# Kernel tuning notes

Hardware: AMD Instinct MI355X
Metric: run time of the kernel (lower is better)

Reference implementation:

```python
import jax, jax.numpy as jnp
import numpy as np

B, N, E, D, H = 128, 256, 1024, 128, 8
DK = D // H
NEG = -9e15

def _xavier(key, shape):
    lim = np.sqrt(6.0 / (shape[0] + shape[1]))
    return jax.random.uniform(key, shape, jnp.float32, -lim, lim)

def setup_inputs() -> dict:
    key = jax.random.key(0)
    ks = jax.random.split(key, 10)
    x = jax.random.normal(ks[0], (B, N, D), jnp.float32)
    mask = jax.random.randint(ks[1], (B, N), 0, 2) > 0
    mask = mask.at[:, 0].set(True)  # ensure no fully-masked molecule
    # unique (row, col) edges per molecule -> scatter .set matches torch index_put
    perm = jax.vmap(lambda k: jax.random.permutation(k, N * N)[:E])(jax.random.split(ks[2], B))
    edge_index = jnp.stack([perm // N, perm % N], axis=1).astype(jnp.int32)  # [B, 2, E]
    edge_attr = jax.random.normal(ks[3], (B, E, D), jnp.float32)
    return {
        "x": x, "mask": mask, "edge_index": edge_index, "edge_attr": edge_attr,
        "Wq": _xavier(ks[4], (D + 2, D)),
        "Wk": _xavier(ks[5], (D + 2, D)),
        "Wv": _xavier(ks[6], (D + 2, D)),
        "We_w": _xavier(ks[7], (D, D)),
        "We_b": jax.random.normal(ks[8], (D,), jnp.float32) * 0.02,
        "ln_g": jnp.ones((D,), jnp.float32),
        "ln_b": jnp.zeros((D,), jnp.float32),
    }

def reference(x, mask, edge_index, edge_attr, Wq, Wk, Wv, We_w, We_b, ln_g, ln_b):
    rows, cols = edge_index[:, 0, :], edge_index[:, 1, :]  # [B, E]
    # per-molecule degree features (torch_geometric.degree per row/col)
    deg = lambda idx: jax.vmap(lambda r: jnp.zeros((N,), x.dtype).at[r].add(1.0))(idx)
    deg_r, deg_c = deg(rows), deg(cols)
    x_new = jnp.concatenate([x, deg_r[..., None], deg_c[..., None]], axis=-1)  # [B,N,D+2]
    # edge bias: linear -> mean over features -> scatter into [B,N,N]
    edge_feats = (edge_attr @ We_w + We_b).mean(axis=-1)  # [B, E]
    edge_bias = jax.vmap(lambda r, c, f: jnp.zeros((N, N), x.dtype).at[r, c].set(f))(rows, cols, edge_feats)
    q = (x_new @ Wq).reshape(B, N, H, DK).transpose(0, 2, 1, 3)
    k = (x_new @ Wk).reshape(B, N, H, DK).transpose(0, 2, 1, 3)
    v = (x_new @ Wv).reshape(B, N, H, DK).transpose(0, 2, 1, 3)
    scores = jnp.einsum('bhqd,bhkd->bhqk', q, k) / np.sqrt(DK).astype(x.dtype)
    # mask keys first, then add edge bias (matches torch op order)
    scores = jnp.where(mask[:, None, None, :], scores, NEG) + edge_bias[:, None, :, :]
    attn = jax.nn.softmax(scores, axis=-1)  # dropout is identity in eval
    out = jnp.einsum('bhqk,bhkd->bhqd', attn, v).transpose(0, 2, 1, 3).reshape(B, N, D)
    out = out + x
    mu = out.mean(axis=-1, keepdims=True)
    var = out.var(axis=-1, keepdims=True)
    return (out - mu) / jnp.sqrt(var + 1e-6) * ln_g + ln_b
```

## Files before the change

kernel.cpp:

```cpp
#include <hip/hip_runtime.h>
#include <stdint.h>

#define NB 128
#define NN 256
#define NE 1024
#define ND 128
#define NH 8
#define NDK 16
#define NEGV -9.0e15f

typedef unsigned short u16;
typedef unsigned int u32;
typedef unsigned char u8;
typedef __attribute__((ext_vector_type(8))) short short8;
typedef __attribute__((ext_vector_type(4))) float float4v;
typedef __attribute__((ext_vector_type(2))) float f32x2;

__device__ __forceinline__ float bf2f(u16 u) { return __uint_as_float(((u32)u) << 16); }
__device__ __forceinline__ u16 f2bf(float f) {
    u32 u = __float_as_uint(f);
    u += 0x7fffu + ((u >> 16) & 1u);
    return (u16)(u >> 16);
}
__device__ __forceinline__ float ldf(const void* p, size_t i, int f32) {
    return f32 ? ((const float*)p)[i] : bf2f(((const u16*)p)[i]);
}
__device__ __forceinline__ void stf(void* p, size_t i, int f32, float v) {
    if (f32) ((float*)p)[i] = v;
    else ((u16*)p)[i] = f2bf(v);
}
__device__ __forceinline__ void unpack8(uint4 a, float* o) {
    o[0] = bf2f(a.x & 0xffff); o[1] = bf2f(a.x >> 16);
    o[2] = bf2f(a.y & 0xffff); o[3] = bf2f(a.y >> 16);
    o[4] = bf2f(a.z & 0xffff); o[5] = bf2f(a.z >> 16);
    o[6] = bf2f(a.w & 0xffff); o[7] = bf2f(a.w >> 16);
}
__device__ __forceinline__ f32x2 bfpair(u32 w) {
    return (f32x2){__uint_as_float(w << 16), __uint_as_float(w & 0xffff0000u)};
}
__device__ __forceinline__ u32 pk_bf(float a, float b) {
    return ((__float_as_uint(a) + 0x8000u) >> 16) |
           ((__float_as_uint(b) + 0x8000u) & 0xffff0000u);
}
union Pack8 { u16 u[8]; u32 w[4]; short8 v; };

__device__ __forceinline__ int wave_detect_f32(const u16* x16) {
    int lane = threadIdx.x & 63;
    uint4 a = *(const uint4*)(x16 + lane * 8);
    u32 w[4] = {a.x, a.y, a.z, a.w};
    u32 ev = 0;
#pragma unroll
    for (int j = 0; j < 4; ++j) {
        ev |= ((((w[j] & 0xffffu) >> 7) & 0xffu) >= 0xC2u) ? 1u : 0u;
        ev |= (((w[j] >> 23) & 0xffu) >= 0xC2u) ? 1u : 0u;
    }
#pragma unroll
    for (int off = 32; off; off >>= 1) ev |= (u32)__shfl_xor((int)ev, off, 64);
    return ev ? 1 : 0;
}
__device__ __forceinline__ int wave_detect_mw(const u8* m8) {
    int lane = threadIdx.x & 63;
    uint4 m = *(const uint4*)(m8 + lane * 16);
    u32 w[4] = {m.x, m.y, m.z, m.w};
    u32 g1 = 0, mx = 0;
#pragma unroll
    for (int j = 0; j < 4; ++j) {
        u32 b0 = w[j] & 0xffu, b1 = (w[j] >> 8) & 0xffu;
        u32 b2 = (w[j] >> 16) & 0xffu, b3 = w[j] >> 24;
        g1 |= b1;
        u32 ma = b0 > b1 ? b0 : b1, mb2 = b2 > b3 ? b2 : b3;
        u32 mc = ma > mb2 ? ma : mb2;
        mx = mx > mc ? mx : mc;
    }
#pragma unroll
    for (int off = 32; off; off >>= 1) {
        g1 |= (u32)__shfl_xor((int)g1, off, 64);
        u32 o = (u32)__shfl_xor((int)mx, off, 64);
        mx = mx > o ? mx : o;
    }
    return (g1 == 0) ? 4 : ((mx <= 1u) ? 1 : 2);
}

__global__ __launch_bounds__(64) void k_wpk(const u16* x16,
                                            const void* Wew, const void* Web,
                                            float* wmean,
                                            const void* Wq, const void* Wk,
                                            const void* Wv, u16* WP) {
    int f32 = wave_detect_f32(x16);
    int bid = blockIdx.x, lane = threadIdx.x;
    if (bid < 129) {
        int k = bid;
        const void* src = (k < 128) ? Wew : Web;
        size_t base = (k < 128) ? (size_t)k * ND : 0;
        float s = ldf(src, base + lane, f32) + ldf(src, base + lane + 64, f32);
#pragma unroll
        for (int off = 32; off; off >>= 1) s += __shfl_xor(s, off, 64);
        if (lane == 0) wmean[k] = s * (1.0f / ND);
    } else {
        int id = bid - 129;
        int kT = id / 24, nT = id % 24;
        int col = lane & 15, quad = lane >> 4;
        int n = nT * 16 + col;
        int mat = n >> 7, nm = n & 127;
        const void* W = (mat == 0) ? Wq : (mat == 1) ? Wk : Wv;
        Pack8 c;
#pragma unroll
        for (int j = 0; j < 8; ++j) {
            int k = kT * 32 + quad * 8 + j;
            c.u[j] = (k < 130) ? f2bf(ldf(W, (size_t)k * ND + nm, f32)) : (u16)0;
        }
        *(short8*)(WP + ((size_t)(kT * 24 + nT) * 64 + lane) * 8) = c.v;
    }
}

__global__ __launch_bounds__(256) void k_edge(const u16* x16, const void* ea,
                                              const float* wmean, const int* ei,
                                              float* degr, float* degc,
                                              int* rowstartG, u16* colsG,
                                              float* featsG) {
    __shared__ __align__(16) float swm[132];
    __shared__ float featsL[NE];
    __shared__ int cr[NN], cc[NN], offs[NN], rs[NN + 1];
    int b = blockIdx.x, tid = threadIdx.x;
    int f32 = wave_detect_f32(x16);
    if (tid <= ND) swm[tid] = wmean[tid];
    cr[tid] = 0; cc[tid] = 0;
    __syncthreads();
    {
        int sub = tid & 15, grp = tid >> 4;
        const float4* wv = (const float4*)&swm[sub * 8];
        float4 w0 = wv[0], w1 = wv[1];
        float wb = swm[ND];
        const size_t ebase = (size_t)b * NE;
#pragma unroll 4
        for (int t = 0; t < 64; ++t) {
            int e = t * 16 + grp;
            size_t base = (ebase + e) * ND + sub * 8;
            float part;
            if (f32) {
                const float4* p = (const float4*)((const float*)ea + base);
                float4 a0 = p[0], a1 = p[1];
                part = a0.x * w0.x + a0.y * w0.y + a0.z * w0.z + a0.w * w0.w +
                       a1.x * w1.x + a1.y * w1.y + a1.z * w1.z + a1.w * w1.w;
            } else {
                uint4 a = *(const uint4*)((const u16*)ea + base);
                float xv[8];
                unpack8(a, xv);
                part = xv[0] * w0.x + xv[1] * w0.y + xv[2] * w0.z + xv[3] * w0.w +
                       xv[4] * w1.x + xv[5] * w1.y + xv[6] * w1.z + xv[7] * w1.w;
            }
            part += __shfl_xor(part, 1);
            part += __shfl_xor(part, 2);
            part += __shfl_xor(part, 4);
            part += __shfl_xor(part, 8);
            if (sub == 0) featsL[e] = part + wb;
        }
    }
    const int* rows = ei + (size_t)b * 2 * NE;
    const int* cols = rows + NE;
    for (int e = tid; e < NE; e += 256) {
        atomicAdd(&cr[rows[e]], 1);
        atomicAdd(&cc[cols[e]], 1);
    }
    __syncthreads();
    degr[b * NN + tid] = (float)cr[tid];
    degc[b * NN + tid] = (float)cc[tid];
    if (tid == 0) {
        int a = 0;
        for (int n = 0; n < NN; ++n) { rs[n] = a; a += cr[n]; }
        rs[NN] = a;
    }
    __syncthreads();
    offs[tid] = rs[tid];
    rowstartG[b * (NN + 1) + tid] = rs[tid];
    if (tid == 0) rowstartG[b * (NN + 1) + NN] = rs[NN];
    __syncthreads();
    for (int e = tid; e < NE; e += 256) {
        int r = rows[e];
        int pos = atomicAdd(&offs[r], 1);
        colsG[(size_t)b * NE + pos] = (u16)cols[e];
        featsG[(size_t)b * NE + pos] = featsL[e];
    }
}

__global__ __launch_bounds__(256) void k_gemm(const void* x, const float* degr,
                                              const float* degc, const u16* WP,
                                              u16* qw, u16* kw,
                                              u16* vw, u16* vt) {
    int tid = threadIdx.x;
    int w = tid >> 6, lane = tid & 63;
    int quad = lane >> 4, col = lane & 15;
    int m0 = blockIdx.x * 64 + w * 16;
    int row = m0 + col;
    int f32 = wave_detect_f32((const u16*)x);

    float4v acc[24];
#pragma unroll
    for (int t = 0; t < 24; ++t) acc[t] = (float4v){0.f, 0.f, 0.f, 0.f};

    const short8* wp = (const short8*)WP;
    for (int kT = 0; kT < 5; ++kT) {
        short8 a;
        if (kT < 4) {
            if (!f32) {
                a = *(const short8*)((const u16*)x + (size_t)row * ND + kT * 32 + quad * 8);
            } else {
                const float* xf = (const float*)x + (size_t)row * ND + kT * 32 + quad * 8;
                Pack8 c;
#pragma unroll
                for (int j = 0; j < 8; ++j) c.u[j] = f2bf(xf[j]);
                a = c.v;
            }
        } else {
            Pack8 c;
#pragma unroll
            for (int j = 0; j < 8; ++j) c.u[j] = 0;
            if (quad == 0) {
                c.u[0] = f2bf(degr[row]);
                c.u[1] = f2bf(degc[row]);
            }
            a = c.v;
        }
#pragma unroll
        for (int nT = 0; nT < 24; ++nT) {
            short8 bfr = wp[(size_t)(kT * 24 + nT) * 64 + lane];
            acc[nT] = __builtin_amdgcn_mfma_f32_16x16x32_bf16(a, bfr, acc[nT], 0, 0, 0);
        }
    }
    int bb = m0 >> 8;
    int nodebase = (m0 & 255) + quad * 4;
#pragma unroll
    for (int nT = 0; nT < 16; ++nT) {
        int h = nT & 7;
        u16* O = (nT < 8) ? qw : kw;
        float sc = (nT < 8) ? 0.25f : 1.0f;
        size_t base = ((size_t)bb * NH + h) * NN + nodebase;
#pragma unroll
        for (int reg = 0; reg < 4; ++reg)
            O[(base + reg) * NDK + col] = f2bf(acc[nT][reg] * sc);
    }
#pragma unroll
    for (int nT = 16; nT < 24; ++nT) {
        int h = nT - 16;
        size_t base = ((size_t)bb * NH + h) * NN + nodebase;
#pragma unroll
        for (int reg = 0; reg < 4; ++reg)
            vw[(base + reg) * NDK + col] = f2bf(acc[nT][reg]);
        u32 lo = (u32)f2bf(acc[nT][0]) | ((u32)f2bf(acc[nT][1]) << 16);
        u32 hi = (u32)f2bf(acc[nT][2]) | ((u32)f2bf(acc[nT][3]) << 16);
        *(uint2*)(vt + (((size_t)bb * NH + h) * NDK + col) * NN + nodebase) = make_uint2(lo, hi);
    }
}

__global__ __launch_bounds__(256, 4) void k_attn(const u16* x16,
                                              const u16* qg, const u16* kg,
                                              const u16* vw, const u16* vt,
                                              const void* mask,
                                              const int* rowstartG, const u16* colsG,
                                              const float* featsG, void* out) {
    __shared__ __align__(16) u16 Ks[NN][24];
    __shared__ __align__(16) u16 Vs[NDK][264];
    __shared__ __align__(16) float mb[NN];
    __shared__ __align__(16) float Of[NN * 17];
    __shared__ float lbuf[NN];
    int h = blockIdx.x, b = blockIdx.y, tid = threadIdx.x;
    int wv = tid >> 6, lane = tid & 63;
    int col = lane & 15, g = lane >> 4;
    int f32 = wave_detect_f32(x16);
    int mw = wave_detect_mw((const u8*)mask);
    size_t hb = ((size_t)b * NH + h) * NN;
    int e0 = rowstartG[b * (NN + 1) + tid];
    int e1 = rowstartG[b * (NN + 1) + tid + 1];
    const uint4* ksrc = (const uint4*)(kg + (hb + tid) * NDK);
    uint4 ka0 = ksrc[0], ka1 = ksrc[1];
    int dk = tid >> 4, chunk = tid & 15;
    const uint4* vsrc = (const uint4*)(vt + ((size_t)(b * NH + h) * NDK + dk) * NN + chunk * 16);
    uint4 va0 = vsrc[0], va1 = vsrc[1];
    bool mv;
    {
        size_t mi = (size_t)b * NN + tid;
        if (mw == 4)      mv = ((const u32*)mask)[mi] != 0;
        else if (mw == 2) mv = ((const u16*)mask)[mi] != 0;
        else              mv = ((const u8*)mask)[mi] != 0;
    }
    f32x2 qr[8];
    {
        const uint4* qp = (const uint4*)(qg + (hb + tid) * NDK);
        uint4 qa_ = qp[0], qb_ = qp[1];
        qr[0] = bfpair(qa_.x); qr[1] = bfpair(qa_.y);
        qr[2] = bfpair(qa_.z); qr[3] = bfpair(qa_.w);
        qr[4] = bfpair(qb_.x); qr[5] = bfpair(qb_.y);
        qr[6] = bfpair(qb_.z); qr[7] = bfpair(qb_.w);
    }
    short8 qf[4];
#pragma unroll
    for (int qt = 0; qt < 4; ++qt) {
        int qtabs = wv * 4 + qt;
        short8 qv = {0, 0, 0, 0, 0, 0, 0, 0};
        if (g < 2)
            qv = *(const short8*)(qg + (hb + qtabs * 16 + col) * NDK + 8 * g);
        qf[qt] = qv;
    }
    {
        uint4* kdst = (uint4*)&Ks[tid][0];
        kdst[0] = ka0; kdst[1] = ka1;
        uint4* vdst = (uint4*)&Vs[dk][chunk * 16];
        vdst[0] = va0; vdst[1] = va1;
        mb[tid] = mv ? 0.0f : NEGV;
    }
    __syncthreads();

    float4v outv[4];
    float lpart[4];
#pragma unroll
    for (int qt = 0; qt < 4; ++qt) {
        outv[qt] = (float4v){0.f, 0.f, 0.f, 0.f};
        lpart[qt] = 0.f;
    }

    for (int kt = 0; kt < 16; ++kt) {
        short8 kf = {0, 0, 0, 0, 0, 0, 0, 0};
        if (g < 2) kf = *(const short8*)&Ks[kt * 16 + col][8 * g];
        Pack8 vv;
        {
            uint2 t2 = *(const uint2*)&Vs[col][kt * 16 + 4 * g];
            vv.w[0] = t2.x; vv.w[1] = t2.y; vv.w[2] = 0; vv.w[3] = 0;
        }
        float4 mb4 = *(const float4*)&mb[kt * 16 + 4 * g];
        float4v cin = (float4v){mb4.x, mb4.y, mb4.z, mb4.w};
#pragma unroll
        for (int qt = 0; qt < 4; ++qt) {
            float4v s4 = __builtin_amdgcn_mfma_f32_16x16x32_bf16(kf, qf[qt], cin, 0, 0, 0);
            float p0 = __expf(fminf(s4[0], 60.f));
            float p1 = __expf(fminf(s4[1], 60.f));
            float p2 = __expf(fminf(s4[2], 60.f));
            float p3 = __expf(fminf(s4[3], 60.f));
            lpart[qt] += (p0 + p1) + (p2 + p3);
            Pack8 pp;
            pp.w[0] = pk_bf(p0, p1);
            pp.w[1] = pk_bf(p2, p3);
            pp.w[2] = 0; pp.w[3] = 0;
            outv[qt] = __builtin_amdgcn_mfma_f32_16x16x32_bf16(pp.v, vv.v, outv[qt], 0, 0, 0);
        }
    }
#pragma unroll
    for (int qt = 0; qt < 4; ++qt) {
        float l = lpart[qt];
        l += __shfl_xor(l, 16);
        l += __shfl_xor(l, 32);
        if (g == 0) lbuf[(wv * 4 + qt) * 16 + col] = l;
        int q0 = (wv * 4 + qt) * 16 + 4 * g;
#pragma unroll
        for (int reg = 0; reg < 4; ++reg)
            Of[(q0 + reg) * 17 + col] = outv[qt][reg];
    }
    __syncthreads();

    float lfin = lbuf[tid];
    f32x2 r[8];
#pragma unroll
    for (int j = 0; j < 8; ++j)
        r[j] = (f32x2){Of[tid * 17 + 2 * j], Of[tid * 17 + 2 * j + 1]};
    if (e0 < e1) {
        const u16* colsB = colsG + (size_t)b * NE;
        const float* featsB = featsG + (size_t)b * NE;
        int c = colsB[e0];
        float f = featsB[e0];
        const uint4* vp0 = (const uint4*)(vw + (hb + c) * NDK);
        uint4 v0 = vp0[0], v1 = vp0[1];
        for (int e = e0; e < e1; ++e) {
            int cc_ = c; float ff_ = f;
            uint4 w0 = v0, w1 = v1;
            if (e + 1 < e1) {
                c = colsB[e + 1];
                f = featsB[e + 1];
                const uint4* vp = (const uint4*)(vw + (hb + c) * NDK);
                v0 = vp[0]; v1 = vp[1];
            }
            const u32* kcw = (const u32*)&Ks[cc_][0];
            f32x2 s2 = qr[0] * bfpair(kcw[0]);
            s2 += qr[1] * bfpair(kcw[1]); s2 += qr[2] * bfpair(kcw[2]);
            s2 += qr[3] * bfpair(kcw[3]); s2 += qr[4] * bfpair(kcw[4]);
            s2 += qr[5] * bfpair(kcw[5]); s2 += qr[6] * bfpair(kcw[6]);
            s2 += qr[7] * bfpair(kcw[7]);
            float s = s2.x + s2.y + mb[cc_];
            float dl = __expf(fminf(s + ff_, 60.f)) - __expf(fminf(s, 60.f));
            lfin += dl;
            f32x2 d2 = (f32x2){dl, dl};
            r[0] += d2 * bfpair(w0.x); r[1] += d2 * bfpair(w0.y);
            r[2] += d2 * bfpair(w0.z); r[3] += d2 * bfpair(w0.w);
            r[4] += d2 * bfpair(w1.x); r[5] += d2 * bfpair(w1.y);
            r[6] += d2 * bfpair(w1.z); r[7] += d2 * bfpair(w1.w);
        }
    }
    float inv = 1.0f / lfin;
    size_t obase = ((size_t)(b * NN + tid)) * ND + h * NDK;
    if (f32) {
        float4* op = (float4*)((float*)out + obase);
#pragma unroll
        for (int jj = 0; jj < 4; ++jj) {
            float4 w;
            w.x = r[2 * jj].x * inv;     w.y = r[2 * jj].y * inv;
            w.z = r[2 * jj + 1].x * inv; w.w = r[2 * jj + 1].y * inv;
            op[jj] = w;
        }
    } else {
        u16* op = (u16*)out + obase;
        Pack8 pa, pb;
#pragma unroll
        for (int jj = 0; jj < 4; ++jj) {
            pa.u[2 * jj]     = f2bf(r[jj].x * inv);
            pa.u[2 * jj + 1] = f2bf(r[jj].y * inv);
            pb.u[2 * jj]     = f2bf(r[jj + 4].x * inv);
            pb.u[2 * jj + 1] = f2bf(r[jj + 4].y * inv);
        }
        *(uint4*)op = *(uint4*)&pa.w[0];
        *(uint4*)(op + 8) = *(uint4*)&pb.w[0];
    }
}

__global__ __launch_bounds__(256) void k_ln(void* out, const void* x, const void* g,
                                            const void* be) {
    int f32 = wave_detect_f32((const u16*)x);
    int tid = threadIdx.x, wv = tid >> 6, lane = tid & 63;
    int row = blockIdx.x * 4 + wv;
    size_t base = (size_t)row * ND;
    float v0 = ldf(out, base + lane, f32) + ldf(x, base + lane, f32);
    float v1 = ldf(out, base + lane + 64, f32) + ldf(x, base + lane + 64, f32);
    float s = v0 + v1, ss = v0 * v0 + v1 * v1;
#pragma unroll
    for (int off = 32; off; off >>= 1) {
        s += __shfl_xor(s, off, 64);
        ss += __shfl_xor(ss, off, 64);
    }
    float mu = s * (1.0f / ND);
    float var = ss * (1.0f / ND) - mu * mu;
    float rs = rsqrtf(var + 1e-6f);
    float o0 = (v0 - mu) * rs * ldf(g, lane, f32) + ldf(be, lane, f32);
    float o1 = (v1 - mu) * rs * ldf(g, lane + 64, f32) + ldf(be, lane + 64, f32);
    stf(out, base + lane, f32, o0);
    stf(out, base + lane + 64, f32, o1);
}

extern "C" void kernel_launch(void* const* d_in, const int* in_sizes, int n_in,
                              void* d_out, int out_size, void* d_ws, size_t ws_size,
                              hipStream_t stream) {
    const void* x = d_in[0];
    const void* mask = d_in[1];
    const int* ei = (const int*)d_in[2];
    const void* ea = d_in[3];
    const void* Wq = d_in[4];
    const void* Wk = d_in[5];
    const void* Wv = d_in[6];
    const void* Wew = d_in[7];
    const void* Web = d_in[8];
    const void* lng = d_in[9];
    const void* lnb = d_in[10];

    char* ws = (char*)d_ws;
    size_t off = 0;
    float* wmean = (float*)(ws + off);   off += 1024;
    float* degr = (float*)(ws + off);    off += (size_t)NB * NN * 4;
    float* degc = (float*)(ws + off);    off += (size_t)NB * NN * 4;
    int* rowstart = (int*)(ws + off);    off += (size_t)NB * (NN + 1) * 4 + 512;
    u16* colsG = (u16*)(ws + off);       off += (size_t)NB * NE * 2;
    float* featsG = (float*)(ws + off);  off += (size_t)NB * NE * 4;
    u16* WP = (u16*)(ws + off);          off += (size_t)5 * 24 * 64 * 8 * 2;
    const size_t qkv_elems = (size_t)NB * NH * NN * NDK;
    u16* qw = (u16*)(ws + off);          off += qkv_elems * 2;
    u16* kw = (u16*)(ws + off);          off += qkv_elems * 2;
    u16* vw = (u16*)(ws + off);          off += qkv_elems * 2;
    u16* vt = (u16*)(ws + off);          off += qkv_elems * 2;

    k_wpk<<<249, 64, 0, stream>>>((const u16*)x, Wew, Web, wmean, Wq, Wk, Wv, WP);
    k_edge<<<NB, 256, 0, stream>>>((const u16*)x, ea, wmean, ei, degr, degc,
                                   rowstart, colsG, featsG);
    k_gemm<<<(NB * NN) / 64, 256, 0, stream>>>(x, degr, degc, WP, qw, kw, vw, vt);
    k_attn<<<dim3(NH, NB), 256, 0, stream>>>((const u16*)x, qw, kw, vw, vt, mask,
                                             rowstart, colsG, featsG, d_out);
    k_ln<<<(NB * NN) / 4, 256, 0, stream>>>(d_out, x, lng, lnb);
}
```

Baseline: 241.0 us.

## Split edge feature projection into wide grid kernel, merge weight prep with CSR build

```diff
diff --git a/kernel.cpp b/kernel.cpp
--- a/kernel.cpp
+++ b/kernel.cpp
@@ -81,81 +81,48 @@
     return (g1 == 0) ? 4 : ((mx <= 1u) ? 1 : 2);
 }
 
-__global__ __launch_bounds__(64) void k_wpk(const u16* x16,
-                                            const void* Wew, const void* Web,
-                                            float* wmean,
-                                            const void* Wq, const void* Wk,
-                                            const void* Wv, u16* WP) {
-    int f32 = wave_detect_f32(x16);
-    int bid = blockIdx.x, lane = threadIdx.x;
-    if (bid < 129) {
-        int k = bid;
-        const void* src = (k < 128) ? Wew : Web;
-        size_t base = (k < 128) ? (size_t)k * ND : 0;
-        float s = ldf(src, base + lane, f32) + ldf(src, base + lane + 64, f32);
-#pragma unroll
-        for (int off = 32; off; off >>= 1) s += __shfl_xor(s, off, 64);
-        if (lane == 0) wmean[k] = s * (1.0f / ND);
-    } else {
-        int id = bid - 129;
-        int kT = id / 24, nT = id % 24;
-        int col = lane & 15, quad = lane >> 4;
-        int n = nT * 16 + col;
-        int mat = n >> 7, nm = n & 127;
-        const void* W = (mat == 0) ? Wq : (mat == 1) ? Wk : Wv;
-        Pack8 c;
-#pragma unroll
-        for (int j = 0; j < 8; ++j) {
-            int k = kT * 32 + quad * 8 + j;
-            c.u[j] = (k < 130) ? f2bf(ldf(W, (size_t)k * ND + nm, f32)) : (u16)0;
-        }
-        *(short8*)(WP + ((size_t)(kT * 24 + nT) * 64 + lane) * 8) = c.v;
-    }
-}
-
-__global__ __launch_bounds__(256) void k_edge(const u16* x16, const void* ea,
-                                              const float* wmean, const int* ei,
-                                              float* degr, float* degc,
-                                              int* rowstartG, u16* colsG,
-                                              float* featsG) {
-    __shared__ __align__(16) float swm[132];
-    __shared__ float featsL[NE];
+__global__ __launch_bounds__(256) void k_pre(const u16* x16,
+                                             const void* Wew, const void* Web,
+                                             float* wmean,
+                                             const void* Wq, const void* Wk,
+                                             const void* Wv, u16* WP,
+                                             const int* ei, float* degr, float* degc,
+                                             int* rowstartG, u16* colsG, u16* posG) {
+    int bid = blockIdx.x, tid = threadIdx.x;
+    if (bid < 249) {
+        if (tid < 64) {
+            int f32 = wave_detect_f32(x16);
+            int lane = tid;
+            if (bid < 129) {
+                int k = bid;
+                const void* src = (k < 128) ? Wew : Web;
+                size_t base = (k < 128) ? (size_t)k * ND : 0;
+                float s = ldf(src, base + lane, f32) + ldf(src, base + lane + 64, f32);
+#pragma unroll
+                for (int off = 32; off; off >>= 1) s += __shfl_xor(s, off, 64);
+                if (lane == 0) wmean[k] = s * (1.0f / ND);
+            } else {
+                int id = bid - 129;
+                int kT = id / 24, nT = id % 24;
+                int col = lane & 15, quad = lane >> 4;
+                int n = nT * 16 + col;
+                int mat = n >> 7, nm = n & 127;
+                const void* W = (mat == 0) ? Wq : (mat == 1) ? Wk : Wv;
+                Pack8 c;
+#pragma unroll
+                for (int j = 0; j < 8; ++j) {
+                    int k = kT * 32 + quad * 8 + j;
+                    c.u[j] = (k < 130) ? f2bf(ldf(W, (size_t)k * ND + nm, f32)) : (u16)0;
+                }
+                *(short8*)(WP + ((size_t)(kT * 24 + nT) * 64 + lane) * 8) = c.v;
+            }
+        }
+        return;
+    }
     __shared__ int cr[NN], cc[NN], offs[NN], rs[NN + 1];
-    int b = blockIdx.x, tid = threadIdx.x;
-    int f32 = wave_detect_f32(x16);
-    if (tid <= ND) swm[tid] = wmean[tid];
+    int b = bid - 249;
     cr[tid] = 0; cc[tid] = 0;
     __syncthreads();
-    {
-        int sub = tid & 15, grp = tid >> 4;
-        const float4* wv = (const float4*)&swm[sub * 8];
-        float4 w0 = wv[0], w1 = wv[1];
-        float wb = swm[ND];
-        const size_t ebase = (size_t)b * NE;
-#pragma unroll 4
-        for (int t = 0; t < 64; ++t) {
-            int e = t * 16 + grp;
-            size_t base = (ebase + e) * ND + sub * 8;
-            float part;
-            if (f32) {
-                const float4* p = (const float4*)((const float*)ea + base);
-                float4 a0 = p[0], a1 = p[1];
-                part = a0.x * w0.x + a0.y * w0.y + a0.z * w0.z + a0.w * w0.w +
-                       a1.x * w1.x + a1.y * w1.y + a1.z * w1.z + a1.w * w1.w;
-            } else {
-                uint4 a = *(const uint4*)((const u16*)ea + base);
-                float xv[8];
-                unpack8(a, xv);
-                part = xv[0] * w0.x + xv[1] * w0.y + xv[2] * w0.z + xv[3] * w0.w +
-                       xv[4] * w1.x + xv[5] * w1.y + xv[6] * w1.z + xv[7] * w1.w;
-            }
-            part += __shfl_xor(part, 1);
-            part += __shfl_xor(part, 2);
-            part += __shfl_xor(part, 4);
-            part += __shfl_xor(part, 8);
-            if (sub == 0) featsL[e] = part + wb;
-        }
-    }
     const int* rows = ei + (size_t)b * 2 * NE;
     const int* cols = rows + NE;
     for (int e = tid; e < NE; e += 256) {
@@ -179,7 +146,44 @@
         int r = rows[e];
         int pos = atomicAdd(&offs[r], 1);
         colsG[(size_t)b * NE + pos] = (u16)cols[e];
-        featsG[(size_t)b * NE + pos] = featsL[e];
+        posG[(size_t)b * NE + e] = (u16)pos;
+    }
+}
+
+__global__ __launch_bounds__(256) void k_efeat(const u16* x16, const void* ea,
+                                               const float* wmean, const u16* posG,
+                                               float* featsG) {
+    __shared__ __align__(16) float swm[132];
+    int tid = threadIdx.x;
+    int f32 = wave_detect_f32(x16);
+    if (tid <= ND) swm[tid] = wmean[tid];
+    __syncthreads();
+    int sub = tid & 15, grp = tid >> 4;
+    size_t eidx = (size_t)blockIdx.x * 16 + grp;
+    const float4* wv = (const float4*)&swm[sub * 8];
+    float4 w0 = wv[0], w1 = wv[1];
+    size_t base = eidx * ND + sub * 8;
+    float part;
+    if (f32) {
+        const float4* p = (const float4*)((const float*)ea + base);
+        float4 a0 = p[0], a1 = p[1];
+        part = a0.x * w0.x + a0.y * w0.y + a0.z * w0.z + a0.w * w0.w +
+               a1.x * w1.x + a1.y * w1.y + a1.z * w1.z + a1.w * w1.w;
+    } else {
+        uint4 a = *(const uint4*)((const u16*)ea + base);
+        float xv[8];
+        unpack8(a, xv);
+        part = xv[0] * w0.x + xv[1] * w0.y + xv[2] * w0.z + xv[3] * w0.w +
+               xv[4] * w1.x + xv[5] * w1.y + xv[6] * w1.z + xv[7] * w1.w;
+    }
+    part += __shfl_xor(part, 1);
+    part += __shfl_xor(part, 2);
+    part += __shfl_xor(part, 4);
+    part += __shfl_xor(part, 8);
+    if (sub == 0) {
+        size_t b = eidx >> 10;
+        int pos = posG[eidx];
+        featsG[b * NE + pos] = part + swm[ND];
     }
 }
 
@@ -464,6 +468,7 @@
     float* degc = (float*)(ws + off);    off += (size_t)NB * NN * 4;
     int* rowstart = (int*)(ws + off);    off += (size_t)NB * (NN + 1) * 4 + 512;
     u16* colsG = (u16*)(ws + off);       off += (size_t)NB * NE * 2;
+    u16* posG = (u16*)(ws + off);        off += (size_t)NB * NE * 2;
     float* featsG = (float*)(ws + off);  off += (size_t)NB * NE * 4;
     u16* WP = (u16*)(ws + off);          off += (size_t)5 * 24 * 64 * 8 * 2;
     const size_t qkv_elems = (size_t)NB * NH * NN * NDK;
@@ -472,9 +477,9 @@
     u16* vw = (u16*)(ws + off);          off += qkv_elems * 2;
     u16* vt = (u16*)(ws + off);          off += qkv_elems * 2;
 
-    k_wpk<<<249, 64, 0, stream>>>((const u16*)x, Wew, Web, wmean, Wq, Wk, Wv, WP);
-    k_edge<<<NB, 256, 0, stream>>>((const u16*)x, ea, wmean, ei, degr, degc,
-                                   rowstart, colsG, featsG);
+    k_pre<<<377, 256, 0, stream>>>((const u16*)x, Wew, Web, wmean, Wq, Wk, Wv, WP,
+                                   ei, degr, degc, rowstart, colsG, posG);
+    k_efeat<<<(NB * NE) / 16, 256, 0, stream>>>((const u16*)x, ea, wmean, posG, featsG);
     k_gemm<<<(NB * NN) / 64, 256, 0, stream>>>(x, degr, degc, WP, qw, kw, vw, vt);
     k_attn<<<dim3(NH, NB), 256, 0, stream>>>((const u16*)x, qw, kw, vw, vt, mask,
                                              rowstart, colsG, featsG, d_out);
```

New measurement: 202.3 us. 16.1% less time.
